# Kernel tuning notes

Hardware: AMD Instinct MI355X
Metric: run time of the kernel (lower is better)

The kernel has to match this reference:

```python
import jax, jax.numpy as jnp
import numpy as np

D_MODEL = 1024
D_STATE = 64
D_HEAD = 64
N_HEADS = 16
D_INNER = D_HEAD * N_HEADS  # 1024
K = 4  # conv kernel size
BATCH = 4
SEQ = 4096
LN_EPS = 1e-5


def setup_inputs() -> dict:
    key = jax.random.key(0)
    k0, k1, k2, k3, k4 = jax.random.split(key, 5)
    x = jax.random.normal(k0, (BATCH, SEQ, D_MODEL), jnp.float32)
    # nn.Linear(d_model, 2*d_inner + 2*d_state, bias=False): weight (out, in)
    in_proj_w = jax.random.normal(k1, (2 * D_INNER + 2 * D_STATE, D_MODEL), jnp.float32) / np.sqrt(D_MODEL).astype(np.float32)
    # depthwise Conv1d: weight (d_inner, 1, K), bias (d_inner,)
    conv_w = jax.random.normal(k2, (D_INNER, 1, K), jnp.float32) * 0.5
    conv_b = jax.random.normal(k3, (D_INNER,), jnp.float32) * 0.1
    # _init_parameters: A = -log(arange(1..d_state)) broadcast to (H, Dh, N)
    A_param = jnp.broadcast_to(-jnp.log(jnp.arange(1, D_STATE + 1, dtype=jnp.float32))[None, None, :],
                               (N_HEADS, D_HEAD, D_STATE))
    ln_w = jnp.ones((D_INNER,), jnp.float32)
    ln_b = jnp.zeros((D_INNER,), jnp.float32)
    out_proj_w = jax.random.normal(k4, (D_MODEL, D_INNER), jnp.float32) / np.sqrt(D_INNER).astype(np.float32)
    return {"x": x, "in_proj_w": in_proj_w, "conv_w": conv_w, "conv_b": conv_b,
            "A_param": A_param, "ln_w": ln_w, "ln_b": ln_b, "out_proj_w": out_proj_w}


def _ssd_scan(xh, Bm, Cm, A_param):
    # xh: (B, L, H, Dh); Bm, Cm: (B, L, N)
    A_disc = jnp.exp(-jnp.exp(A_param))  # (H, Dh, N)

    def step(h, inp):
        x_t, B_t, C_t = inp  # (B,H,Dh), (B,N), (B,N)
        h = h * A_disc + B_t[:, None, None, :] * x_t[..., None]  # (B,H,Dh,N)
        y_t = jnp.einsum('bhdn,bn->bhd', h, C_t)
        return h, y_t

    b = xh.shape[0]
    h0 = jnp.zeros((b, N_HEADS, D_HEAD, D_STATE), xh.dtype)
    xs = (jnp.swapaxes(xh, 0, 1), jnp.swapaxes(Bm, 0, 1), jnp.swapaxes(Cm, 0, 1))
    _, ys = jax.lax.scan(step, h0, xs)  # ys: (L, B, H, Dh)
    return jnp.swapaxes(ys, 0, 1)  # (B, L, H, Dh)


def reference(x, in_proj_w, conv_w, conv_b, A_param, ln_w, ln_b, out_proj_w):
    b, L, _ = x.shape
    xBC = x @ in_proj_w.T  # (B, L, 2*d_inner + 2*d_state)
    xc = xBC[..., :D_INNER]
    z = xBC[..., D_INNER:2 * D_INNER]
    Bm = xBC[..., 2 * D_INNER:2 * D_INNER + D_STATE]
    Cm = xBC[..., 2 * D_INNER + D_STATE:]
    # causal depthwise conv (padding=3 then truncate == left-pad K-1)
    xt = jnp.swapaxes(xc, 1, 2)  # (B, C, L)
    y = jax.lax.conv_general_dilated(xt, conv_w, window_strides=(1,), padding=[(K - 1, 0)],
                                     feature_group_count=D_INNER,
                                     dimension_numbers=('NCH', 'OIH', 'NCH'))
    xc = jnp.swapaxes(y + conv_b[None, :, None], 1, 2)  # (B, L, d_inner)
    xc = jax.nn.silu(xc)
    xh = xc.reshape(b, L, N_HEADS, D_HEAD)
    yssd = _ssd_scan(xh, Bm, Cm, A_param).reshape(b, L, D_INNER)
    yg = yssd * jax.nn.silu(z)
    mu = yg.mean(-1, keepdims=True)
    var = yg.var(-1, keepdims=True)
    yn = (yg - mu) / jnp.sqrt(var + LN_EPS) * ln_w + ln_b
    return yn @ out_proj_w.T
```

## Files before the change

### kernel.cpp

```cpp
#include <hip/hip_runtime.h>

typedef unsigned short u16;
typedef unsigned int u32;
typedef __attribute__((ext_vector_type(8))) short bf16x8;
typedef __attribute__((ext_vector_type(4))) float f32x4;

#define BATCH 4
#define SEQ 4096
#define DMODEL 1024
#define DINNER 1024
#define NPROJ 2176
#define MROWS (BATCH*SEQ)
#define NCHUNK 64
#define CLEN 64
#define NPAD 2304

__device__ __forceinline__ float bf2f(u16 u) {
    union { u32 i; float f; } v; v.i = ((u32)u) << 16; return v.f;
}
__device__ __forceinline__ u16 f2bf(float f) {
    union { float f; u32 i; } v; v.f = f;
    u32 r = v.i + 0x7FFFu + ((v.i >> 16) & 1u);
    return (u16)(r >> 16);
}
__device__ __forceinline__ float silu_f(float x) { return x / (1.0f + expf(-x)); }

__device__ __forceinline__ void gload8f(const u16* p, float* o) {
    bf16x8 v = *(const bf16x8*)p;
    #pragma unroll
    for (int j = 0; j < 8; ++j) o[j] = bf2f((u16)v[j]);
}

__device__ __forceinline__ void ld_lds16(const u16* g, u16* l) {
    __builtin_amdgcn_global_load_lds(
        (const __attribute__((address_space(1))) u32*)g,
        (__attribute__((address_space(3))) u32*)l, 16, 0, 0);
}

__global__ __launch_bounds__(256) void cast_f2b(
    const float* __restrict__ src, u16* __restrict__ dst, int n8)
{
    int i = blockIdx.x * 256 + threadIdx.x;
    if (i >= n8) return;
    size_t o = (size_t)i * 8;
    float4 a = *(const float4*)(src + o);
    float4 b = *(const float4*)(src + o + 4);
    u16 v[8] = {f2bf(a.x), f2bf(a.y), f2bf(a.z), f2bf(a.w),
                f2bf(b.x), f2bf(b.y), f2bf(b.z), f2bf(b.w)};
    *(bf16x8*)(dst + o) = *(bf16x8*)v;
}

__global__ __launch_bounds__(256) void cast_w1p_k(
    const float* __restrict__ src, u16* __restrict__ dst)
{
    int i = blockIdx.x * 256 + threadIdx.x;
    int row = i >> 7;
    size_t o = (size_t)i * 8;
    u16 v[8];
    if (row < NPROJ) {
        float4 a = *(const float4*)(src + o);
        float4 b = *(const float4*)(src + o + 4);
        v[0]=f2bf(a.x); v[1]=f2bf(a.y); v[2]=f2bf(a.z); v[3]=f2bf(a.w);
        v[4]=f2bf(b.x); v[5]=f2bf(b.y); v[6]=f2bf(b.z); v[7]=f2bf(b.w);
    } else {
        #pragma unroll
        for (int j = 0; j < 8; ++j) v[j] = 0;
    }
    *(bf16x8*)(dst + o) = *(bf16x8*)v;
}

__global__ __launch_bounds__(256) void tables_k(
    const float* __restrict__ A_param, float* __restrict__ l2a_g,
    float* __restrict__ apw, float* __restrict__ ainv)
{
    __shared__ float l2s[64];
    int tid = threadIdx.x;
    if (tid < 64) {
        float v = -expf(A_param[tid]) * 1.44269504088896340736f;
        l2s[tid] = v;
        l2a_g[tid] = v;
    }
    __syncthreads();
    #pragma unroll
    for (int i = 0; i < 16; ++i) {
        int e = tid * 16 + i;
        int t = e >> 6, n = e & 63;
        float x = (float)t * l2s[n];
        apw[e]  = exp2f(x);
        ainv[e] = exp2f(-x);
    }
}

#define GK 1024
#define GNT 16

template<typename TO, int GN, int NV, int LDC>
__global__ __launch_bounds__(512, 2) void gemm8p_k(
    const u16* __restrict__ A, const u16* __restrict__ B, TO* __restrict__ C)
{
    __shared__ u16 lds[65536];

    const int cpx = (GN * 64) >> 3;
    const int bid = blockIdx.x;
    const int swz = (bid & 7) * cpx + (bid >> 3);
    const int bm = swz / GN, bn = swz % GN;
    const int m0 = bm * 256, n0 = bn * 256;

    const int tid = threadIdx.x;
    const int wid = tid >> 6, lane = tid & 63;
    const int wm = wid >> 2, wn = wid & 3;
    const int quad = lane >> 4, l16 = lane & 15;
    const int xsw = (l16 & 7) << 3;

    u16* L = lds;
    const u16* Ab = A + (size_t)m0 * GK;
    const u16* Bb = B + (size_t)n0 * GK;

    auto stage = [&](const u16* gbase, u16* ldsb) {
        {
            int c = tid;
            int row = c >> 3, slot = (c & 7) ^ (row & 7);
            ld_lds16(gbase + (size_t)row * GK + slot * 8,
                     ldsb + ((tid & ~63) << 3));
        }
        {
            int c = 512 + tid;
            int row = c >> 3, slot = (c & 7) ^ (row & 7);
            ld_lds16(gbase + (size_t)row * GK + slot * 8,
                     ldsb + ((512 + (tid & ~63)) << 3));
        }
    };
    auto rdfrag = [&](const u16* base, int rh, int kh) -> bf16x8 {
        return *(const bf16x8*)(base + rh * 64 + ((kh * 32 + quad * 8) ^ xsw));
    };

    bf16x8 aLo[4][2], aHi[4][2], bLo[2][2], bHi[2][2];
    f32x4 acc[8][4] = {};

    stage(Ab,                     L);
    stage(Ab + 128 * GK,          L + 8192);
    stage(Bb,                     L + 32768);
    stage(Bb + 128 * GK,          L + 40960);
    stage(Ab + 64,                L + 16384);
    stage(Ab + 128 * GK + 64,     L + 24576);
    asm volatile("s_waitcnt vmcnt(4)" ::: "memory");
    __builtin_amdgcn_s_barrier();
    {
        const u16* Ard = L + wm * 8192;
        #pragma unroll
        for (int i = 0; i < 4; ++i)
            #pragma unroll
            for (int kh = 0; kh < 2; ++kh)
                aLo[i][kh] = rdfrag(Ard, i * 16 + l16, kh);
    }

    for (int t = 0; t < GNT; ++t) {
        const int cb = t & 1;
        u16* Acur = L + cb * 16384;
        u16* Anxt = L + (cb ^ 1) * 16384;
        u16* Bnxt = L + 32768 + (cb ^ 1) * 16384;
        const u16* ArdC = Acur + wm * 8192;
        const u16* ArdN = Anxt + wm * 8192;
        const u16* BrdC = L + 32768 + cb * 16384 + (wn >> 1) * 8192;
        const int brh = (wn & 1) * 64;

        #pragma unroll
        for (int j = 0; j < 2; ++j)
            #pragma unroll
            for (int kh = 0; kh < 2; ++kh)
                bLo[j][kh] = rdfrag(BrdC, brh + j * 16 + l16, kh);
        if (t + 1 < GNT) stage(Bb + (t + 1) * 64, Bnxt);
        __builtin_amdgcn_s_barrier();
        asm volatile("s_waitcnt lgkmcnt(0)" ::: "memory");
        __builtin_amdgcn_s_setprio(1);
        #pragma unroll
        for (int kh = 0; kh < 2; ++kh)
            #pragma unroll
            for (int i = 0; i < 4; ++i)
                #pragma unroll
                for (int j = 0; j < 2; ++j)
                    acc[i][j] = __builtin_amdgcn_mfma_f32_16x16x32_bf16(
                        aLo[i][kh], bLo[j][kh], acc[i][j], 0, 0, 0);
        __builtin_amdgcn_s_setprio(0);
        __builtin_amdgcn_s_barrier();

        #pragma unroll
        for (int j = 0; j < 2; ++j)
            #pragma unroll
            for (int kh = 0; kh < 2; ++kh)
                bHi[j][kh] = rdfrag(BrdC, brh + 32 + j * 16 + l16, kh);
        if (t + 1 < GNT) stage(Bb + 128 * GK + (t + 1) * 64, Bnxt + 8192);
        __builtin_amdgcn_s_barrier();
        asm volatile("s_waitcnt lgkmcnt(0)" ::: "memory");
        __builtin_amdgcn_s_setprio(1);
        #pragma unroll
        for (int kh = 0; kh < 2; ++kh)
            #pragma unroll
            for (int i = 0; i < 4; ++i)
                #pragma unroll
                for (int j = 0; j < 2; ++j)
                    acc[i][2 + j] = __builtin_amdgcn_mfma_f32_16x16x32_bf16(
                        aLo[i][kh], bHi[j][kh], acc[i][2 + j], 0, 0, 0);
        __builtin_amdgcn_s_setprio(0);
        __builtin_amdgcn_s_barrier();

        #pragma unroll
        for (int i = 0; i < 4; ++i)
            #pragma unroll
            for (int kh = 0; kh < 2; ++kh)
                aHi[i][kh] = rdfrag(ArdC, 64 + i * 16 + l16, kh);
        if (t + 2 < GNT) stage(Ab + (t + 2) * 64, Acur);
        if (t + 2 < GNT)      { asm volatile("s_waitcnt vmcnt(6)" ::: "memory"); }
        else if (t + 1 < GNT) { asm volatile("s_waitcnt vmcnt(4)" ::: "memory"); }
        __builtin_amdgcn_s_barrier();
        asm volatile("s_waitcnt lgkmcnt(0)" ::: "memory");
        __builtin_amdgcn_s_setprio(1);
        #pragma unroll
        for (int kh = 0; kh < 2; ++kh)
            #pragma unroll
            for (int i = 0; i < 4; ++i)
                #pragma unroll
                for (int j = 0; j < 2; ++j)
                    acc[4 + i][2 + j] = __builtin_amdgcn_mfma_f32_16x16x32_bf16(
                        aHi[i][kh], bHi[j][kh], acc[4 + i][2 + j], 0, 0, 0);
        __builtin_amdgcn_s_setprio(0);
        __builtin_amdgcn_s_barrier();

        if (t + 1 < GNT) {
            #pragma unroll
            for (int i = 0; i < 4; ++i)
                #pragma unroll
                for (int kh = 0; kh < 2; ++kh)
                    aLo[i][kh] = rdfrag(ArdN, i * 16 + l16, kh);
        }
        if (t + 2 < GNT) stage(Ab + 128 * GK + (t + 2) * 64, Acur + 8192);
        if (t + 2 < GNT)      { asm volatile("s_waitcnt vmcnt(4)" ::: "memory"); }
        else if (t + 1 < GNT) { asm volatile("s_waitcnt vmcnt(0)" ::: "memory"); }
        __builtin_amdgcn_s_barrier();
        asm volatile("s_waitcnt lgkmcnt(0)" ::: "memory");
        __builtin_amdgcn_s_setprio(1);
        #pragma unroll
        for (int kh = 0; kh < 2; ++kh)
            #pragma unroll
            for (int i = 0; i < 4; ++i)
                #pragma unroll
                for (int j = 0; j < 2; ++j)
                    acc[4 + i][j] = __builtin_amdgcn_mfma_f32_16x16x32_bf16(
                        aHi[i][kh], bLo[j][kh], acc[4 + i][j], 0, 0, 0);
        __builtin_amdgcn_s_setprio(0);
        __builtin_amdgcn_s_barrier();
    }

    __syncthreads();
    if constexpr (sizeof(TO) == 2) {
        u16* eld = lds;
        #pragma unroll
        for (int i = 0; i < 8; ++i)
            #pragma unroll
            for (int j = 0; j < 4; ++j)
                #pragma unroll
                for (int r = 0; r < 4; ++r)
                    eld[(size_t)(wm * 128 + i * 16 + quad * 4 + r) * 256 +
                        wn * 64 + j * 16 + l16] = f2bf(acc[i][j][r]);
        __syncthreads();
        #pragma unroll
        for (int rep = 0; rep < 16; ++rep) {
            int cc = rep * 512 + tid;
            int row = cc >> 5, c8 = (cc & 31) * 8;
            if (n0 + c8 < NV)
                *(bf16x8*)(C + (size_t)(m0 + row) * LDC + n0 + c8) =
                    *(const bf16x8*)(eld + (size_t)row * 256 + c8);
        }
    } else {
        float* eldf = (float*)lds;
        #pragma unroll
        for (int h = 0; h < 2; ++h) {
            if (wm == h) {
                #pragma unroll
                for (int i = 0; i < 8; ++i)
                    #pragma unroll
                    for (int j = 0; j < 4; ++j)
                        #pragma unroll
                        for (int r = 0; r < 4; ++r)
                            eldf[(size_t)(i * 16 + quad * 4 + r) * 256 +
                                 wn * 64 + j * 16 + l16] = acc[i][j][r];
            }
            __syncthreads();
            #pragma unroll
            for (int rep = 0; rep < 16; ++rep) {
                int cc = rep * 512 + tid;
                int row = cc >> 6, c4 = (cc & 63) * 4;
                *(float4*)(C + (size_t)(m0 + h * 128 + row) * LDC + n0 + c4) =
                    *(const float4*)(eldf + (size_t)row * 256 + c4);
            }
            __syncthreads();
        }
    }
}

#define CRPT 8
__global__ __launch_bounds__(256) void conv_k(
    const u16* __restrict__ xBC, const float* __restrict__ conv_w,
    const float* __restrict__ conv_b, u16* __restrict__ xact)
{
    int o = blockIdx.x * 256 + threadIdx.x;
    int c0 = (o & 127) * 8;
    int rg = o >> 7;
    int row0 = rg * CRPT;
    int l0 = row0 & (SEQ - 1);

    float4 wv[8];
    #pragma unroll
    for (int j = 0; j < 8; ++j)
        wv[j] = *(const float4*)(conv_w + (c0 + j) * 4);
    float bias[8];
    {
        float4 b0 = *(const float4*)(conv_b + c0);
        float4 b1 = *(const float4*)(conv_b + c0 + 4);
        bias[0]=b0.x; bias[1]=b0.y; bias[2]=b0.z; bias[3]=b0.w;
        bias[4]=b1.x; bias[5]=b1.y; bias[6]=b1.z; bias[7]=b1.w;
    }

    float win[3][8];
    #pragma unroll
    for (int k = 0; k < 3; ++k) {
        if (l0 - 3 + k < 0) {
            #pragma unroll
            for (int j = 0; j < 8; ++j) win[k][j] = 0.f;
        } else {
            gload8f(xBC + (size_t)(row0 - 3 + k) * NPROJ + c0, win[k]);
        }
    }
    #pragma unroll
    for (int r = 0; r < CRPT; ++r) {
        float cur[8];
        gload8f(xBC + (size_t)(row0 + r) * NPROJ + c0, cur);
        u16 outv[8];
        #pragma unroll
        for (int j = 0; j < 8; ++j) {
            float acc = bias[j]
                + win[0][j] * wv[j].x + win[1][j] * wv[j].y
                + win[2][j] * wv[j].z + cur[j]    * wv[j].w;
            outv[j] = f2bf(silu_f(acc));
        }
        *(bf16x8*)(xact + (size_t)(row0 + r) * DINNER + c0) = *(bf16x8*)outv;
        #pragma unroll
        for (int j = 0; j < 8; ++j) {
            win[0][j] = win[1][j]; win[1][j] = win[2][j]; win[2][j] = cur[j];
        }
    }
}

__global__ __launch_bounds__(256) void ssd_intra_k(
    const u16* __restrict__ xact, u16* __restrict__ xBC,
    float* __restrict__ S, const float* __restrict__ apw,
    const float* __restrict__ ainv)
{
    __shared__ u16 Pl[64][72];
    __shared__ u16 Ql[64][72];
    __shared__ u16 Gl[64][72];
    __shared__ u16 Qt[64][72];
    __shared__ u16 Xt[64][72];

    const int dg = blockIdx.x, c = blockIdx.y, b = blockIdx.z;
    const int dcol = dg * 64;
    const int l0 = c * CLEN;
    const int tid = threadIdx.x;
    const int w = tid >> 6, lane = tid & 63;
    const int quad = lane >> 4, l16 = lane & 15;
    const int tstrip = 16 * w;

    {
        const int st_t = tid >> 3, st_n8 = (tid & 7) * 8;
        #pragma unroll
        for (int rep = 0; rep < 2; ++rep) {
            int t = rep * 32 + st_t;
            size_t row = (size_t)(b * SEQ + l0 + t) * NPROJ;
            float Bv[8], Cv[8];
            gload8f(xBC + row + 2048 + st_n8, Bv);
            gload8f(xBC + row + 2112 + st_n8, Cv);
            float4 aw0 = *(const float4*)&apw[t * 64 + st_n8];
            float4 aw1 = *(const float4*)&apw[t * 64 + st_n8 + 4];
            float4 ai0 = *(const float4*)&ainv[t * 64 + st_n8];
            float4 ai1 = *(const float4*)&ainv[t * 64 + st_n8 + 4];
            float4 ar0 = *(const float4*)&apw[(63 - t) * 64 + st_n8];
            float4 ar1 = *(const float4*)&apw[(63 - t) * 64 + st_n8 + 4];
            float aw[8] = {aw0.x,aw0.y,aw0.z,aw0.w,aw1.x,aw1.y,aw1.z,aw1.w};
            float ai[8] = {ai0.x,ai0.y,ai0.z,ai0.w,ai1.x,ai1.y,ai1.z,ai1.w};
            float ar[8] = {ar0.x,ar0.y,ar0.z,ar0.w,ar1.x,ar1.y,ar1.z,ar1.w};
            u16 p8[8], q8[8];
            #pragma unroll
            for (int j = 0; j < 8; ++j) {
                p8[j] = f2bf(Cv[j] * aw[j]);
                q8[j] = f2bf(Bv[j] * ai[j]);
            }
            *(bf16x8*)&Pl[t][st_n8] = *(bf16x8*)p8;
            *(bf16x8*)&Ql[t][st_n8] = *(bf16x8*)q8;
            #pragma unroll
            for (int j = 0; j < 8; ++j)
                Qt[st_n8 + j][t] = f2bf(Bv[j] * ar[j]);
        }
    }
    {
        #pragma unroll
        for (int rep = 0; rep < 2; ++rep) {
            int idx = rep * 256 + tid;
            int xt_t = idx >> 3, xt_d8 = (idx & 7) * 8;
            float xv[8];
            gload8f(xact + (size_t)(b * SEQ + l0 + xt_t) * DINNER + dcol + xt_d8, xv);
            #pragma unroll
            for (int j = 0; j < 8; ++j) Xt[xt_d8 + j][xt_t] = f2bf(xv[j]);
        }
    }
    __syncthreads();

    bf16x8 af0 = *(const bf16x8*)&Pl[tstrip + l16][0  + quad * 8];
    bf16x8 af1 = *(const bf16x8*)&Pl[tstrip + l16][32 + quad * 8];
    f32x4 g[4] = {};
    #pragma unroll
    for (int j4 = 0; j4 < 4; ++j4) {
        bf16x8 b0 = *(const bf16x8*)&Ql[j4 * 16 + l16][0  + quad * 8];
        bf16x8 b1 = *(const bf16x8*)&Ql[j4 * 16 + l16][32 + quad * 8];
        g[j4] = __builtin_amdgcn_mfma_f32_16x16x32_bf16(af0, b0, g[j4], 0, 0, 0);
        g[j4] = __builtin_amdgcn_mfma_f32_16x16x32_bf16(af1, b1, g[j4], 0, 0, 0);
    }
    __syncthreads();

    #pragma unroll
    for (int j4 = 0; j4 < 4; ++j4) {
        #pragma unroll
        for (int r = 0; r < 4; ++r) {
            int t = tstrip + quad * 4 + r;
            int s = j4 * 16 + l16;
            float val = (s <= t) ? g[j4][r] : 0.f;
            u16 hi = f2bf(val);
            Ql[t][s] = hi;
            Gl[t][s] = f2bf(val - bf2f(hi));
        }
    }
    __syncthreads();

    bf16x8 gh0 = *(const bf16x8*)&Ql[tstrip + l16][0  + quad * 8];
    bf16x8 gh1 = *(const bf16x8*)&Ql[tstrip + l16][32 + quad * 8];
    bf16x8 gl0 = *(const bf16x8*)&Gl[tstrip + l16][0  + quad * 8];
    bf16x8 gl1 = *(const bf16x8*)&Gl[tstrip + l16][32 + quad * 8];
    bf16x8 qt0 = *(const bf16x8*)&Qt[tstrip + l16][0  + quad * 8];
    bf16x8 qt1 = *(const bf16x8*)&Qt[tstrip + l16][32 + quad * 8];

    #pragma unroll
    for (int dt = 0; dt < 4; ++dt) {
        bf16x8 x0 = *(const bf16x8*)&Xt[dt * 16 + l16][0  + quad * 8];
        bf16x8 x1 = *(const bf16x8*)&Xt[dt * 16 + l16][32 + quad * 8];
        f32x4 y = {};
        y = __builtin_amdgcn_mfma_f32_16x16x32_bf16(gh0, x0, y, 0, 0, 0);
        y = __builtin_amdgcn_mfma_f32_16x16x32_bf16(gh1, x1, y, 0, 0, 0);
        y = __builtin_amdgcn_mfma_f32_16x16x32_bf16(gl0, x0, y, 0, 0, 0);
        y = __builtin_amdgcn_mfma_f32_16x16x32_bf16(gl1, x1, y, 0, 0, 0);
        f32x4 s4 = {};
        s4 = __builtin_amdgcn_mfma_f32_16x16x32_bf16(qt0, x0, s4, 0, 0, 0);
        s4 = __builtin_amdgcn_mfma_f32_16x16x32_bf16(qt1, x1, s4, 0, 0, 0);
        #pragma unroll
        for (int r = 0; r < 4; ++r) {
            int t = tstrip + quad * 4 + r;
            xBC[(size_t)(b * SEQ + l0 + t) * NPROJ + dcol + dt * 16 + l16] = f2bf(y[r]);
            int n = tstrip + quad * 4 + r;
            S[((size_t)((b * NCHUNK + c) * 64 + n)) * 1024 + dcol + dt * 16 + l16] = s4[r];
        }
    }
}

__global__ __launch_bounds__(256) void state_scan_k(
    float* __restrict__ S, const float* __restrict__ l2a)
{
    int gid = blockIdx.x * 256 + threadIdx.x;
    int b = gid >> 16, r = gid & 65535, n = r >> 10;
    float a64 = exp2f(64.f * l2a[n]);
    float v = 0.f;
    size_t base = ((size_t)b << 22) + r;
    for (int c = 0; c < NCHUNK; ++c) {
        size_t addr = base + ((size_t)c << 16);
        float s = S[addr];
        S[addr] = v;
        v = fmaf(v, a64, s);
    }
}

__global__ __launch_bounds__(256) void ssd_inter_k(
    u16* __restrict__ xBC, const float* __restrict__ S,
    const float* __restrict__ apw, const float* __restrict__ l2a)
{
    __shared__ u16 Pl[64][72];
    __shared__ u16 Vt[64][72];

    const int dg = blockIdx.x, c = blockIdx.y, b = blockIdx.z;
    const int dcol = dg * 64;
    const int l0 = c * CLEN;
    const int tid = threadIdx.x;
    const int w = tid >> 6, lane = tid & 63;
    const int quad = lane >> 4, l16 = lane & 15;
    const int tstrip = 16 * w;

    {
        const int st_t = tid >> 3, st_n8 = (tid & 7) * 8;
        #pragma unroll
        for (int rep = 0; rep < 2; ++rep) {
            int t = rep * 32 + st_t;
            float Cv[8];
            gload8f(xBC + (size_t)(b * SEQ + l0 + t) * NPROJ + 2112 + st_n8, Cv);
            float4 aw0 = *(const float4*)&apw[t * 64 + st_n8];
            float4 aw1 = *(const float4*)&apw[t * 64 + st_n8 + 4];
            float aw[8] = {aw0.x,aw0.y,aw0.z,aw0.w,aw1.x,aw1.y,aw1.z,aw1.w};
            u16 p8[8];
            #pragma unroll
            for (int j = 0; j < 8; ++j) p8[j] = f2bf(Cv[j] * aw[j]);
            *(bf16x8*)&Pl[t][st_n8] = *(bf16x8*)p8;
        }
    }
    {
        #pragma unroll
        for (int rep = 0; rep < 2; ++rep) {
            int idx = rep * 256 + tid;
            int vn = idx >> 3, vd8 = (idx & 7) * 8;
            float an = exp2f(l2a[vn]);
            const float* vp = S + ((size_t)((b * NCHUNK + c) * 64 + vn)) * 1024 + dcol + vd8;
            float4 v0 = *(const float4*)vp;
            float4 v1 = *(const float4*)(vp + 4);
            float vv[8] = {v0.x,v0.y,v0.z,v0.w,v1.x,v1.y,v1.z,v1.w};
            #pragma unroll
            for (int j = 0; j < 8; ++j) Vt[vd8 + j][vn] = f2bf(an * vv[j]);
        }
    }
    __syncthreads();

    bf16x8 af0 = *(const bf16x8*)&Pl[tstrip + l16][0  + quad * 8];
    bf16x8 af1 = *(const bf16x8*)&Pl[tstrip + l16][32 + quad * 8];
    #pragma unroll
    for (int dt = 0; dt < 4; ++dt) {
        bf16x8 hb0 = *(const bf16x8*)&Vt[dt * 16 + l16][0  + quad * 8];
        bf16x8 hb1 = *(const bf16x8*)&Vt[dt * 16 + l16][32 + quad * 8];
        f32x4 y = {};
        y = __builtin_amdgcn_mfma_f32_16x16x32_bf16(af0, hb0, y, 0, 0, 0);
        y = __builtin_amdgcn_mfma_f32_16x16x32_bf16(af1, hb1, y, 0, 0, 0);
        #pragma unroll
        for (int r = 0; r < 4; ++r) {
            int t = tstrip + quad * 4 + r;
            size_t addr = (size_t)(b * SEQ + l0 + t) * NPROJ + dcol + dt * 16 + l16;
            xBC[addr] = f2bf(bf2f(xBC[addr]) + y[r]);
        }
    }
}

__global__ __launch_bounds__(256) void gate_k(
    const u16* __restrict__ xBC, const float* __restrict__ ln_w,
    const float* __restrict__ ln_b, u16* __restrict__ yn)
{
    __shared__ float r1[4], r2[4];
    const int row = blockIdx.x;
    const int tid = threadIdx.x;
    const int lane = tid & 63, wid = tid >> 6;
    const size_t base = (size_t)row * NPROJ;

    float gv[4];
    {
        const ushort4 yv = *(const ushort4*)(xBC + base + tid * 4);
        const ushort4 zv = *(const ushort4*)(xBC + base + 1024 + tid * 4);
        gv[0] = bf2f(yv.x) * silu_f(bf2f(zv.x));
        gv[1] = bf2f(yv.y) * silu_f(bf2f(zv.y));
        gv[2] = bf2f(yv.z) * silu_f(bf2f(zv.z));
        gv[3] = bf2f(yv.w) * silu_f(bf2f(zv.w));
    }
    float ps = gv[0] + gv[1] + gv[2] + gv[3];
    float pq = gv[0]*gv[0] + gv[1]*gv[1] + gv[2]*gv[2] + gv[3]*gv[3];
    #pragma unroll
    for (int off = 1; off < 64; off <<= 1) {
        ps += __shfl_xor(ps, off);
        pq += __shfl_xor(pq, off);
    }
    if (lane == 0) { r1[wid] = ps; r2[wid] = pq; }
    __syncthreads();
    float ts = r1[0] + r1[1] + r1[2] + r1[3];
    float tq = r2[0] + r2[1] + r2[2] + r2[3];
    float mu = ts * (1.0f / DINNER);
    float var = tq * (1.0f / DINNER) - mu * mu;
    float inv = rsqrtf(var + 1e-5f);

    u16 outv[4];
    #pragma unroll
    for (int j = 0; j < 4; ++j) {
        int c = tid * 4 + j;
        float v = (gv[j] - mu) * inv * ln_w[c] + ln_b[c];
        outv[j] = f2bf(v);
    }
    *(ushort4*)(yn + (size_t)row * DINNER + tid * 4) = *(ushort4*)outv;
}

extern "C" void kernel_launch(void* const* d_in, const int* in_sizes, int n_in,
                              void* d_out, int out_size, void* d_ws, size_t ws_size,
                              hipStream_t stream) {
    const float* x   = (const float*)d_in[0];
    const float* w1  = (const float*)d_in[1];
    const float* cw  = (const float*)d_in[2];
    const float* cb  = (const float*)d_in[3];
    const float* ap  = (const float*)d_in[4];
    const float* lnw = (const float*)d_in[5];
    const float* lnb = (const float*)d_in[6];
    const float* w2  = (const float*)d_in[7];
    float* out = (float*)d_out;

    u16* xBC   = (u16*)d_ws;
    u16* xact  = xBC + (size_t)MROWS * NPROJ;
    u16* x_bf  = xact;
    u16* w2_bf = xact + (size_t)MROWS * DINNER;
    float* l2a  = (float*)(w2_bf + (size_t)DMODEL * DINNER);
    float* apw  = l2a + 64;
    float* ainv = apw + 4096;
    u16*   w1p = (u16*)d_out;
    float* S   = (float*)d_out;

    cast_f2b<<<(MROWS * DMODEL / 8) / 256, 256, 0, stream>>>(x, x_bf, MROWS * DMODEL / 8);
    cast_w1p_k<<<(NPAD * DMODEL / 8) / 256, 256, 0, stream>>>(w1, w1p);
    cast_f2b<<<(DMODEL * DINNER / 8) / 256, 256, 0, stream>>>(w2, w2_bf, DMODEL * DINNER / 8);
    tables_k<<<1, 256, 0, stream>>>(ap, l2a, apw, ainv);

    gemm8p_k<u16, 9, NPROJ, NPROJ><<<9 * 64, 512, 0, stream>>>(x_bf, w1p, xBC);
    conv_k<<<(MROWS / CRPT * 128) / 256, 256, 0, stream>>>(xBC, cw, cb, xact);

    ssd_intra_k<<<dim3(16, NCHUNK, BATCH), 256, 0, stream>>>(xact, xBC, S, apw, ainv);
    state_scan_k<<<1024, 256, 0, stream>>>(S, l2a);
    ssd_inter_k<<<dim3(16, NCHUNK, BATCH), 256, 0, stream>>>(xBC, S, apw, l2a);

    gate_k<<<MROWS, 256, 0, stream>>>(xBC, lnw, lnb, xact);
    gemm8p_k<float, 4, DMODEL, DMODEL><<<4 * 64, 512, 0, stream>>>(xact, w2_bf, out);
}
```

Measured before the change: 385.4 us.

## Fuse inter-chunk SSD pass with gating and LayerNorm; store chunk states in bf16

Merges the inter-chunk state contribution and the gate/LayerNorm kernel into one kernel that handles a full 64-row chunk across all 1024 channels. This removes the read-modify-write of y in xBC and the separate gate pass. Chunk states S are also stored as bf16 instead of fp32, halving state traffic in the intra, scan and inter kernels. In exchange the scan carries are rounded to bf16, which costs accuracy, and the fused kernel has only 256 blocks with large LDS use (about 140KB), so occupancy is low.

```diff
diff --git a/kernel.cpp b/kernel.cpp
--- a/kernel.cpp
+++ b/kernel.cpp
@@ -353,7 +353,7 @@
 
 __global__ __launch_bounds__(256) void ssd_intra_k(
     const u16* __restrict__ xact, u16* __restrict__ xBC,
-    float* __restrict__ S, const float* __restrict__ apw,
+    u16* __restrict__ Sh, const float* __restrict__ apw,
     const float* __restrict__ ainv)
 {
     __shared__ u16 Pl[64][72];
@@ -464,13 +464,13 @@
             int t = tstrip + quad * 4 + r;
             xBC[(size_t)(b * SEQ + l0 + t) * NPROJ + dcol + dt * 16 + l16] = f2bf(y[r]);
             int n = tstrip + quad * 4 + r;
-            S[((size_t)((b * NCHUNK + c) * 64 + n)) * 1024 + dcol + dt * 16 + l16] = s4[r];
+            Sh[((size_t)((b * NCHUNK + c) * 64 + n)) * 1024 + dcol + dt * 16 + l16] = f2bf(s4[r]);
         }
     }
 }
 
 __global__ __launch_bounds__(256) void state_scan_k(
-    float* __restrict__ S, const float* __restrict__ l2a)
+    u16* __restrict__ Sh, const float* __restrict__ l2a)
 {
     int gid = blockIdx.x * 256 + threadIdx.x;
     int b = gid >> 16, r = gid & 65535, n = r >> 10;
@@ -479,119 +479,148 @@
     size_t base = ((size_t)b << 22) + r;
     for (int c = 0; c < NCHUNK; ++c) {
         size_t addr = base + ((size_t)c << 16);
-        float s = S[addr];
-        S[addr] = v;
+        float s = bf2f(Sh[addr]);
+        Sh[addr] = f2bf(v);
         v = fmaf(v, a64, s);
     }
 }
 
-__global__ __launch_bounds__(256) void ssd_inter_k(
-    u16* __restrict__ xBC, const float* __restrict__ S,
-    const float* __restrict__ apw, const float* __restrict__ l2a)
+__global__ __launch_bounds__(512, 2) void inter_gate_k(
+    const u16* __restrict__ xBC, const u16* __restrict__ Sh,
+    const float* __restrict__ apw, const float* __restrict__ l2a,
+    const float* __restrict__ ln_w, const float* __restrict__ ln_b,
+    u16* __restrict__ yn)
 {
     __shared__ u16 Pl[64][72];
-    __shared__ u16 Vt[64][72];
-
-    const int dg = blockIdx.x, c = blockIdx.y, b = blockIdx.z;
-    const int dcol = dg * 64;
-    const int l0 = c * CLEN;
+    __shared__ u16 Vt[1024][68];
+    __shared__ float red[64][8][2];
+    __shared__ float stats[64][2];
+
+    const int c = blockIdx.x, b = blockIdx.y;
     const int tid = threadIdx.x;
     const int w = tid >> 6, lane = tid & 63;
     const int quad = lane >> 4, l16 = lane & 15;
-    const int tstrip = 16 * w;
+    const int dW = w * 128;
+    const int brow = b * SEQ + c * CLEN;
 
     {
         const int st_t = tid >> 3, st_n8 = (tid & 7) * 8;
+        float Cv[8];
+        gload8f(xBC + (size_t)(brow + st_t) * NPROJ + 2112 + st_n8, Cv);
+        float4 aw0 = *(const float4*)&apw[st_t * 64 + st_n8];
+        float4 aw1 = *(const float4*)&apw[st_t * 64 + st_n8 + 4];
+        float aw[8] = {aw0.x,aw0.y,aw0.z,aw0.w,aw1.x,aw1.y,aw1.z,aw1.w};
+        u16 p8[8];
+        #pragma unroll
+        for (int j = 0; j < 8; ++j)
+            p8[j] = f2bf(Cv[j] * aw[j] * exp2f(l2a[st_n8 + j]));
+        *(bf16x8*)&Pl[st_t][st_n8] = *(bf16x8*)p8;
+    }
+    {
+        const size_t vbase = (size_t)((b * NCHUNK + c) * 64) * 1024;
+        const int n0 = (tid & 7) * 8;
         #pragma unroll
         for (int rep = 0; rep < 2; ++rep) {
-            int t = rep * 32 + st_t;
-            float Cv[8];
-            gload8f(xBC + (size_t)(b * SEQ + l0 + t) * NPROJ + 2112 + st_n8, Cv);
-            float4 aw0 = *(const float4*)&apw[t * 64 + st_n8];
-            float4 aw1 = *(const float4*)&apw[t * 64 + st_n8 + 4];
-            float aw[8] = {aw0.x,aw0.y,aw0.z,aw0.w,aw1.x,aw1.y,aw1.z,aw1.w};
-            u16 p8[8];
-            #pragma unroll
-            for (int j = 0; j < 8; ++j) p8[j] = f2bf(Cv[j] * aw[j]);
-            *(bf16x8*)&Pl[t][st_n8] = *(bf16x8*)p8;
-        }
-    }
-    {
-        #pragma unroll
-        for (int rep = 0; rep < 2; ++rep) {
-            int idx = rep * 256 + tid;
-            int vn = idx >> 3, vd8 = (idx & 7) * 8;
-            float an = exp2f(l2a[vn]);
-            const float* vp = S + ((size_t)((b * NCHUNK + c) * 64 + vn)) * 1024 + dcol + vd8;
-            float4 v0 = *(const float4*)vp;
-            float4 v1 = *(const float4*)(vp + 4);
-            float vv[8] = {v0.x,v0.y,v0.z,v0.w,v1.x,v1.y,v1.z,v1.w};
-            #pragma unroll
-            for (int j = 0; j < 8; ++j) Vt[vd8 + j][vn] = f2bf(an * vv[j]);
-        }
-    }
-    __syncthreads();
-
-    bf16x8 af0 = *(const bf16x8*)&Pl[tstrip + l16][0  + quad * 8];
-    bf16x8 af1 = *(const bf16x8*)&Pl[tstrip + l16][32 + quad * 8];
-    #pragma unroll
-    for (int dt = 0; dt < 4; ++dt) {
-        bf16x8 hb0 = *(const bf16x8*)&Vt[dt * 16 + l16][0  + quad * 8];
-        bf16x8 hb1 = *(const bf16x8*)&Vt[dt * 16 + l16][32 + quad * 8];
-        f32x4 y = {};
-        y = __builtin_amdgcn_mfma_f32_16x16x32_bf16(af0, hb0, y, 0, 0, 0);
-        y = __builtin_amdgcn_mfma_f32_16x16x32_bf16(af1, hb1, y, 0, 0, 0);
+            int d_blk = (tid >> 3) + rep * 64;
+            bf16x8 vin[8];
+            #pragma unroll
+            for (int jj = 0; jj < 8; ++jj)
+                vin[jj] = *(const bf16x8*)&Sh[vbase + (size_t)(n0 + jj) * 1024 + d_blk * 8];
+            #pragma unroll
+            for (int jj2 = 0; jj2 < 8; ++jj2) {
+                u16 outv[8];
+                #pragma unroll
+                for (int jj = 0; jj < 8; ++jj) outv[jj] = (u16)vin[jj][jj2];
+                *(bf16x8*)&Vt[d_blk * 8 + jj2][n0] = *(bf16x8*)outv;
+            }
+        }
+    }
+    __syncthreads();
+
+    bf16x8 pa[4][2];
+    #pragma unroll
+    for (int i = 0; i < 4; ++i)
+        #pragma unroll
+        for (int kh = 0; kh < 2; ++kh)
+            pa[i][kh] = *(const bf16x8*)&Pl[i * 16 + l16][kh * 32 + quad * 8];
+
+    f32x4 acc[4][8] = {};
+    #pragma unroll
+    for (int j = 0; j < 8; ++j) {
+        bf16x8 pb0 = *(const bf16x8*)&Vt[dW + j * 16 + l16][quad * 8];
+        bf16x8 pb1 = *(const bf16x8*)&Vt[dW + j * 16 + l16][32 + quad * 8];
+        #pragma unroll
+        for (int i = 0; i < 4; ++i) {
+            acc[i][j] = __builtin_amdgcn_mfma_f32_16x16x32_bf16(pa[i][0], pb0, acc[i][j], 0, 0, 0);
+            acc[i][j] = __builtin_amdgcn_mfma_f32_16x16x32_bf16(pa[i][1], pb1, acc[i][j], 0, 0, 0);
+        }
+    }
+
+    float s1[4][4] = {}, s2[4][4] = {};
+    #pragma unroll
+    for (int i = 0; i < 4; ++i)
+        #pragma unroll
+        for (int j = 0; j < 8; ++j)
+            #pragma unroll
+            for (int r = 0; r < 4; ++r) {
+                int t = i * 16 + quad * 4 + r;
+                size_t rb = (size_t)(brow + t) * NPROJ;
+                int d = dW + j * 16 + l16;
+                float yo = bf2f(xBC[rb + d]);
+                float zz = bf2f(xBC[rb + 1024 + d]);
+                float gq = (yo + acc[i][j][r]) * silu_f(zz);
+                acc[i][j][r] = gq;
+                s1[i][r] += gq;
+                s2[i][r] += gq * gq;
+            }
+
+    #pragma unroll
+    for (int i = 0; i < 4; ++i)
         #pragma unroll
         for (int r = 0; r < 4; ++r) {
-            int t = tstrip + quad * 4 + r;
-            size_t addr = (size_t)(b * SEQ + l0 + t) * NPROJ + dcol + dt * 16 + l16;
-            xBC[addr] = f2bf(bf2f(xBC[addr]) + y[r]);
-        }
-    }
-}
-
-__global__ __launch_bounds__(256) void gate_k(
-    const u16* __restrict__ xBC, const float* __restrict__ ln_w,
-    const float* __restrict__ ln_b, u16* __restrict__ yn)
-{
-    __shared__ float r1[4], r2[4];
-    const int row = blockIdx.x;
-    const int tid = threadIdx.x;
-    const int lane = tid & 63, wid = tid >> 6;
-    const size_t base = (size_t)row * NPROJ;
-
-    float gv[4];
-    {
-        const ushort4 yv = *(const ushort4*)(xBC + base + tid * 4);
-        const ushort4 zv = *(const ushort4*)(xBC + base + 1024 + tid * 4);
-        gv[0] = bf2f(yv.x) * silu_f(bf2f(zv.x));
-        gv[1] = bf2f(yv.y) * silu_f(bf2f(zv.y));
-        gv[2] = bf2f(yv.z) * silu_f(bf2f(zv.z));
-        gv[3] = bf2f(yv.w) * silu_f(bf2f(zv.w));
-    }
-    float ps = gv[0] + gv[1] + gv[2] + gv[3];
-    float pq = gv[0]*gv[0] + gv[1]*gv[1] + gv[2]*gv[2] + gv[3]*gv[3];
-    #pragma unroll
-    for (int off = 1; off < 64; off <<= 1) {
-        ps += __shfl_xor(ps, off);
-        pq += __shfl_xor(pq, off);
-    }
-    if (lane == 0) { r1[wid] = ps; r2[wid] = pq; }
-    __syncthreads();
-    float ts = r1[0] + r1[1] + r1[2] + r1[3];
-    float tq = r2[0] + r2[1] + r2[2] + r2[3];
-    float mu = ts * (1.0f / DINNER);
-    float var = tq * (1.0f / DINNER) - mu * mu;
-    float inv = rsqrtf(var + 1e-5f);
-
-    u16 outv[4];
-    #pragma unroll
-    for (int j = 0; j < 4; ++j) {
-        int c = tid * 4 + j;
-        float v = (gv[j] - mu) * inv * ln_w[c] + ln_b[c];
-        outv[j] = f2bf(v);
-    }
-    *(ushort4*)(yn + (size_t)row * DINNER + tid * 4) = *(ushort4*)outv;
+            float a = s1[i][r], q = s2[i][r];
+            #pragma unroll
+            for (int off = 1; off < 16; off <<= 1) {
+                a += __shfl_xor(a, off);
+                q += __shfl_xor(q, off);
+            }
+            if (l16 == 0) {
+                int t = i * 16 + quad * 4 + r;
+                red[t][w][0] = a;
+                red[t][w][1] = q;
+            }
+        }
+    __syncthreads();
+    if (tid < 64) {
+        float ts = 0.f, tq = 0.f;
+        #pragma unroll
+        for (int ww = 0; ww < 8; ++ww) { ts += red[tid][ww][0]; tq += red[tid][ww][1]; }
+        float mu = ts * (1.0f / DINNER);
+        float var = tq * (1.0f / DINNER) - mu * mu;
+        stats[tid][0] = mu;
+        stats[tid][1] = rsqrtf(var + 1e-5f);
+    }
+    __syncthreads();
+
+    float lw[8], lb[8];
+    #pragma unroll
+    for (int j = 0; j < 8; ++j) {
+        lw[j] = ln_w[dW + j * 16 + l16];
+        lb[j] = ln_b[dW + j * 16 + l16];
+    }
+    #pragma unroll
+    for (int i = 0; i < 4; ++i)
+        #pragma unroll
+        for (int r = 0; r < 4; ++r) {
+            int t = i * 16 + quad * 4 + r;
+            float mu = stats[t][0], inv = stats[t][1];
+            size_t ob = (size_t)(brow + t) * DINNER;
+            #pragma unroll
+            for (int j = 0; j < 8; ++j) {
+                int d = dW + j * 16 + l16;
+                yn[ob + d] = f2bf((acc[i][j][r] - mu) * inv * lw[j] + lb[j]);
+            }
+        }
 }
 
 extern "C" void kernel_launch(void* const* d_in, const int* in_sizes, int n_in,
@@ -614,8 +643,8 @@
     float* l2a  = (float*)(w2_bf + (size_t)DMODEL * DINNER);
     float* apw  = l2a + 64;
     float* ainv = apw + 4096;
-    u16*   w1p = (u16*)d_out;
-    float* S   = (float*)d_out;
+    u16* w1p = (u16*)d_out;
+    u16* Sh  = (u16*)d_out;
 
     cast_f2b<<<(MROWS * DMODEL / 8) / 256, 256, 0, stream>>>(x, x_bf, MROWS * DMODEL / 8);
     cast_w1p_k<<<(NPAD * DMODEL / 8) / 256, 256, 0, stream>>>(w1, w1p);
@@ -625,10 +654,9 @@
     gemm8p_k<u16, 9, NPROJ, NPROJ><<<9 * 64, 512, 0, stream>>>(x_bf, w1p, xBC);
     conv_k<<<(MROWS / CRPT * 128) / 256, 256, 0, stream>>>(xBC, cw, cb, xact);
 
-    ssd_intra_k<<<dim3(16, NCHUNK, BATCH), 256, 0, stream>>>(xact, xBC, S, apw, ainv);
-    state_scan_k<<<1024, 256, 0, stream>>>(S, l2a);
-    ssd_inter_k<<<dim3(16, NCHUNK, BATCH), 256, 0, stream>>>(xBC, S, apw, l2a);
-
-    gate_k<<<MROWS, 256, 0, stream>>>(xBC, lnw, lnb, xact);
+    ssd_intra_k<<<dim3(16, NCHUNK, BATCH), 256, 0, stream>>>(xact, xBC, Sh, apw, ainv);
+    state_scan_k<<<1024, 256, 0, stream>>>(Sh, l2a);
+    inter_gate_k<<<dim3(NCHUNK, BATCH), 512, 0, stream>>>(xBC, Sh, apw, l2a, lnw, lnb, xact);
+
     gemm8p_k<float, 4, DMODEL, DMODEL><<<4 * 64, 512, 0, stream>>>(xact, w2_bf, out);
 }
```

New measurement: 428.2 us. 11.1% more time.
